# Optimization experiments

Hardware: AMD Instinct MI355X
Metric: run time of the kernel (lower is better)

## Reference

```python
import jax, jax.numpy as jnp
import numpy as np

V, B, N, D, L, H = 30522, 32, 512, 512, 4, 8
HD = D // H
REC = L // 2  # block-recurrent layer index
SCALE = HD ** -0.5


def _ln(x, g, b):
    m = x.mean(-1, keepdims=True)
    v = ((x - m) ** 2).mean(-1, keepdims=True)
    return (x - m) / jnp.sqrt(v + 1e-5) * g + b


def _rope(t):
    # t: [b,h,n,hd]; rotary embedding on token positions (split-half convention)
    n = t.shape[2]
    inv = 1.0 / (10000.0 ** (jnp.arange(0, HD, 2, dtype=jnp.float32) / HD))
    f = jnp.arange(n, dtype=jnp.float32)[:, None] * inv  # [n, hd/2]
    cos, sin = jnp.cos(f), jnp.sin(f)
    t1, t2 = t[..., : HD // 2], t[..., HD // 2 :]
    return jnp.concatenate([t1 * cos - t2 * sin, t2 * cos + t1 * sin], -1)


def _heads(x):
    b, n, _ = x.shape
    return x.reshape(b, n, H, HD).transpose(0, 2, 1, 3)


def _merge(x):
    b, h, n, d = x.shape
    return x.transpose(0, 2, 1, 3).reshape(b, n, h * d)


def _attn(q, k, v, mask):
    s = jnp.einsum('bhid,bhjd->bhij', q, k) * SCALE
    if mask is not None:
        s = jnp.where(mask, s, jnp.float32(-1e9))
    a = jax.nn.softmax(s, axis=-1)
    return jnp.einsum('bhij,bhjd->bhid', a, v)


def setup_inputs() -> dict:
    key = jax.random.key(0)
    ks = jax.random.split(key, 12)
    w = lambda k, shp: jax.random.normal(k, shp, jnp.float32) * 0.02
    return {
        'ids': jax.random.randint(ks[0], (B, N), 0, V),
        'state': jax.random.normal(ks[1], (B, D), jnp.float32),
        'tok_emb': w(ks[2], (V, D)),
        'ln1_g': jnp.ones((L, D), jnp.float32), 'ln1_b': jnp.zeros((L, D), jnp.float32),
        'w_qkv': w(ks[3], (L, D, 3 * D)),
        'w_o': w(ks[4], (L, D, D)),
        'ln2_g': jnp.ones((L, D), jnp.float32), 'ln2_b': jnp.zeros((L, D), jnp.float32),
        'w_ff1': w(ks[5], (L, D, 4 * D)), 'b_ff1': jnp.zeros((L, 4 * D), jnp.float32),
        'w_ff2': w(ks[6], (L, 4 * D, D)), 'b_ff2': jnp.zeros((L, D), jnp.float32),
        's_ln_g': jnp.ones((D,), jnp.float32), 's_ln_b': jnp.zeros((D,), jnp.float32),
        'w_s_qkv': w(ks[7], (D, 3 * D)),
        'w_so': w(ks[8], (D, D)),
        'gate_beta': w(ks[9], (D,)),
        'f_ln_g': jnp.ones((D,), jnp.float32), 'f_ln_b': jnp.zeros((D,), jnp.float32),
        'head_w': w(ks[10], (D, 1)), 'head_b': jnp.zeros((1,), jnp.float32),
    }


def reference(ids, state, tok_emb, ln1_g, ln1_b, w_qkv, w_o, ln2_g, ln2_b,
              w_ff1, b_ff1, w_ff2, b_ff2, s_ln_g, s_ln_b, w_s_qkv, w_so,
              gate_beta, f_ln_g, f_ln_b, head_w, head_b):
    x = tok_emb[ids]                       # [b,n,d]
    s = state[:, None, :]                  # [b,1,d]  (state.unsqueeze(1))
    n = x.shape[1]
    causal = jnp.tril(jnp.ones((n, n), bool))
    for l in range(L):
        h = _ln(x, ln1_g[l], ln1_b[l])
        q, k, v = jnp.split(h @ w_qkv[l], 3, axis=-1)
        q, k, v = _heads(q), _heads(k), _heads(v)
        q, k = _rope(q), _rope(k)
        if l == REC:
            sn = _ln(s, s_ln_g, s_ln_b)
            sq, sk, sv = jnp.split(sn @ w_s_qkv, 3, axis=-1)
            sq, sk, sv = _heads(sq), _heads(sk), _heads(sv)
            # tokens attend over [tokens (causal), state vector (always visible)]
            m = jnp.concatenate([causal, jnp.ones((n, 1), bool)], axis=1)
            out_x = _attn(q, jnp.concatenate([k, sk], 2), jnp.concatenate([v, sv], 2), m)
            x = x + _merge(out_x) @ w_o[l]
            # state attends over [state, all tokens] (no mask)
            out_s = _attn(sq, jnp.concatenate([sk, k], 2), jnp.concatenate([sv, v], 2), None)
            upd = _merge(out_s) @ w_so
            g = jax.nn.sigmoid(gate_beta)   # fixed learned-EMA gate
            s = s * g + upd * (1.0 - g)
        else:
            out_x = _attn(q, k, v, causal)
            x = x + _merge(out_x) @ w_o[l]
        h2 = _ln(x, ln2_g[l], ln2_b[l])
        x = x + jax.nn.gelu(h2 @ w_ff1[l] + b_ff1[l]) @ w_ff2[l] + b_ff2[l]
    x = _ln(x, f_ln_g, f_ln_b)
    state_out = s[:, 0, :]                 # state[0].squeeze()
    logits = x @ head_w + head_b           # [b,n,1]
    out = jax.nn.log_softmax(logits, axis=-1)
    return out, state_out
```

## Files before the change

kernel.cpp:

```cpp
#include <hip/hip_runtime.h>
#include <hip/hip_bf16.h>
#include <math.h>

#define B_ 32
#define N_ 512
#define D_ 512
#define H_ 8
#define HD_ 64
#define QKV_ 1536
#define SCALE_ 0.125f

typedef unsigned short u16;
typedef unsigned int u32;
typedef __attribute__((ext_vector_type(8))) short bf16x8;
typedef __attribute__((ext_vector_type(4))) float f32x4;

#define GLOBAL_AS __attribute__((address_space(1)))
#define LDS_AS __attribute__((address_space(3)))

__device__ __forceinline__ float gelu_f(float x) {
  float u = 0.7978845608028654f * (x + 0.044715f * x * x * x);
  u = fminf(fmaxf(u, -15.f), 15.f);
  float e = __expf(2.f * u);
  float th = 1.f - 2.f * __builtin_amdgcn_rcpf(e + 1.f);
  return 0.5f * x * (1.0f + th);
}

__device__ __forceinline__ u16 f2b(float f) {
  union { float f; u32 u; } v;
  v.f = f;
  u32 r = (v.u + 0x7FFFu + ((v.u >> 16) & 1u)) >> 16;
  return (u16)r;
}

__device__ __forceinline__ float b2f(u16 x) {
  union { u32 u; float f; } v;
  v.u = ((u32)x) << 16;
  return v.f;
}

__device__ __forceinline__ int xcd_swz(int orig, int nwg) {
  int q = nwg >> 3, r = nwg & 7;
  int xcd = orig & 7, idx = orig >> 3;
  return (xcd < r ? xcd * (q + 1) : r * (q + 1) + (xcd - r) * q) + idx;
}

__global__ void k_prep(const float* __restrict__ w_qkv, const float* __restrict__ w_o,
                       const float* __restrict__ w_ff1, const float* __restrict__ w_ff2,
                       u16* __restrict__ wq_t, u16* __restrict__ wo_t,
                       u16* __restrict__ wf1_t, u16* __restrict__ wf2_t,
                       float* __restrict__ out0, float2* __restrict__ tab) {
  __shared__ float tile[32][33];
  int bid = blockIdx.x;
  int t = threadIdx.x;
  if (bid < 64) {
    int idx = bid * 256 + t;
    out0[idx] = 0.f;
    int n = idx >> 5, i = idx & 31;
    float inv = powf(10000.0f, -(float)i * (1.0f / 32.0f));
    float f = (float)n * inv;
    float s, c;
    sincosf(f, &s, &c);
    tab[idx] = make_float2(c, s);
    return;
  }
  int b2 = bid - 64;
  const float* W;
  u16* Wt;
  int K, N;
  if (b2 < 2304) {
    int l = b2 / 768; b2 -= l * 768;
    W = w_qkv + (size_t)l * D_ * QKV_; Wt = wq_t + (size_t)l * QKV_ * D_;
    K = D_; N = QKV_;
  } else if (b2 < 2816) {
    b2 -= 2304; int l = b2 >> 8; b2 &= 255;
    W = w_o + (size_t)l * D_ * D_; Wt = wo_t + (size_t)l * D_ * D_;
    K = D_; N = D_;
  } else if (b2 < 4864) {
    b2 -= 2816; int l = b2 >> 10; b2 &= 1023;
    W = w_ff1 + (size_t)l * D_ * 4 * D_; Wt = wf1_t + (size_t)l * 4 * D_ * D_;
    K = D_; N = 4 * D_;
  } else {
    b2 -= 4864; int l = b2 >> 10; b2 &= 1023;
    W = w_ff2 + (size_t)l * 4 * D_ * D_; Wt = wf2_t + (size_t)l * D_ * 4 * D_;
    K = 4 * D_; N = D_;
  }
  int nbx = N >> 5;
  int bx = b2 % nbx, by = b2 / nbx;
  int k0 = by * 32, n0 = bx * 32;
  int r = t >> 3, c4 = (t & 7) * 4;
  float4 v = *(const float4*)&W[(size_t)(k0 + r) * N + n0 + c4];
  tile[r][c4] = v.x; tile[r][c4 + 1] = v.y; tile[r][c4 + 2] = v.z; tile[r][c4 + 3] = v.w;
  __syncthreads();
  ushort4 o;
  o.x = f2b(tile[c4 + 0][r]); o.y = f2b(tile[c4 + 1][r]);
  o.z = f2b(tile[c4 + 2][r]); o.w = f2b(tile[c4 + 3][r]);
  *(ushort4*)&Wt[(size_t)(n0 + r) * K + k0 + c4] = o;
}

__global__ void k_embed(const int* __restrict__ ids, const float* __restrict__ emb,
                        float* __restrict__ x) {
  int row = blockIdx.x;
  int id = ids[row];
  const float4* s = (const float4*)(emb + (size_t)id * D_);
  float4* d = (float4*)(x + (size_t)row * D_);
  d[threadIdx.x] = s[threadIdx.x];
}

template <int BF16OUT>
__global__ void k_ln(const float* __restrict__ in, const float* __restrict__ gw,
                     const float* __restrict__ bw, void* __restrict__ outv) {
  int row = blockIdx.x * 4 + (threadIdx.x >> 6);
  int lane = threadIdx.x & 63;
  const float* p = in + (size_t)row * D_ + lane * 8;
  float4 v0 = *(const float4*)p;
  float4 v1 = *(const float4*)(p + 4);
  float s = v0.x + v0.y + v0.z + v0.w + v1.x + v1.y + v1.z + v1.w;
  float q = v0.x * v0.x + v0.y * v0.y + v0.z * v0.z + v0.w * v0.w +
            v1.x * v1.x + v1.y * v1.y + v1.z * v1.z + v1.w * v1.w;
#pragma unroll
  for (int o = 32; o >= 1; o >>= 1) {
    s += __shfl_xor(s, o);
    q += __shfl_xor(q, o);
  }
  float mean = s * (1.0f / D_);
  float var = q * (1.0f / D_) - mean * mean;
  float rstd = rsqrtf(var + 1e-5f);
  float4 g0 = *(const float4*)(gw + lane * 8);
  float4 g1 = *(const float4*)(gw + lane * 8 + 4);
  float4 b0 = *(const float4*)(bw + lane * 8);
  float4 b1 = *(const float4*)(bw + lane * 8 + 4);
  float o8[8];
  o8[0] = (v0.x - mean) * rstd * g0.x + b0.x;
  o8[1] = (v0.y - mean) * rstd * g0.y + b0.y;
  o8[2] = (v0.z - mean) * rstd * g0.z + b0.z;
  o8[3] = (v0.w - mean) * rstd * g0.w + b0.w;
  o8[4] = (v1.x - mean) * rstd * g1.x + b1.x;
  o8[5] = (v1.y - mean) * rstd * g1.y + b1.y;
  o8[6] = (v1.z - mean) * rstd * g1.z + b1.z;
  o8[7] = (v1.w - mean) * rstd * g1.w + b1.w;
  if (BF16OUT) {
    u16* op = (u16*)outv + (size_t)row * D_ + lane * 8;
    ushort4 a, b;
    a.x = f2b(o8[0]); a.y = f2b(o8[1]); a.z = f2b(o8[2]); a.w = f2b(o8[3]);
    b.x = f2b(o8[4]); b.y = f2b(o8[5]); b.z = f2b(o8[6]); b.w = f2b(o8[7]);
    *(ushort4*)op = a;
    *(ushort4*)(op + 4) = b;
  } else {
    float* op = (float*)outv + (size_t)row * D_ + lane * 8;
    *(float4*)op = make_float4(o8[0], o8[1], o8[2], o8[3]);
    *(float4*)(op + 4) = make_float4(o8[4], o8[5], o8[6], o8[7]);
  }
}

template <int EPI, int BF16OUT>
__global__ __launch_bounds__(256) void k_mgemm(
    const u16* __restrict__ A, const u16* __restrict__ Bt,
    const float* __restrict__ bias, const float* __restrict__ resid,
    void* __restrict__ Cv, int M, int K, int Nc, int nb0) {
  __shared__ u16 As[2][128 * 32];
  __shared__ u16 Bs[2][128 * 32];
  int t = threadIdx.x;
  int wave = t >> 6, lane = t & 63;
  int nwg = gridDim.x * gridDim.y;
  int swz = xcd_swz(blockIdx.y * gridDim.x + blockIdx.x, nwg);
  int m0 = (swz / gridDim.x) * 128;
  int n0 = ((swz % gridDim.x) + nb0) * 128;
  int wr = wave >> 1, wc = wave & 1;
  f32x4 acc[4][4] = {};

  int srow = lane >> 2;
  int scol = ((lane & 3) ^ ((lane >> 3) & 3)) * 8;
  const u16* gaBase = A + (size_t)(m0 + wave * 32 + srow) * K + scol;
  const u16* gbBase = Bt + (size_t)(n0 + wave * 32 + srow) * K + scol;

#define STAGE_MG(bsel, kk)                                                     \
  {                                                                            \
    _Pragma("unroll") for (int i_ = 0; i_ < 2; ++i_) {                         \
      int rbase_ = wave * 32 + i_ * 16;                                        \
      __builtin_amdgcn_global_load_lds(                                        \
          (const GLOBAL_AS void*)(gaBase + (size_t)(i_ * 16) * K + (kk)),      \
          (LDS_AS void*)&As[bsel][rbase_ * 32], 16, 0, 0);                     \
      __builtin_amdgcn_global_load_lds(                                        \
          (const GLOBAL_AS void*)(gbBase + (size_t)(i_ * 16) * K + (kk)),      \
          (LDS_AS void*)&Bs[bsel][rbase_ * 32], 16, 0, 0);                     \
    }                                                                          \
  }

  int c = lane & 15, g = lane >> 4;
  int rsw = (c >> 1) & 3;
  int chread = (g ^ rsw) * 8;

  int nIter = K >> 5;
  STAGE_MG(0, 0);
  __syncthreads();
  for (int it = 0; it < nIter; ++it) {
    int cur = it & 1;
    if (it + 1 < nIter) STAGE_MG(cur ^ 1, (it + 1) << 5);
    const u16* as = As[cur];
    const u16* bs = Bs[cur];
    bf16x8 af[4], bfr[4];
#pragma unroll
    for (int mi = 0; mi < 4; ++mi)
      af[mi] = *(const bf16x8*)&as[(wr * 64 + mi * 16 + c) * 32 + chread];
#pragma unroll
    for (int ni = 0; ni < 4; ++ni)
      bfr[ni] = *(const bf16x8*)&bs[(wc * 64 + ni * 16 + c) * 32 + chread];
#pragma unroll
    for (int mi = 0; mi < 4; ++mi)
#pragma unroll
      for (int ni = 0; ni < 4; ++ni)
        acc[mi][ni] = __builtin_amdgcn_mfma_f32_16x16x32_bf16(bfr[ni], af[mi], acc[mi][ni], 0, 0, 0);
    __syncthreads();
  }
#undef STAGE_MG

#pragma unroll
  for (int mi = 0; mi < 4; ++mi) {
    int m = m0 + wr * 64 + mi * 16 + (lane & 15);
    size_t rowoff = (size_t)m * Nc;
#pragma unroll
    for (int ni = 0; ni < 4; ++ni) {
      int n = n0 + wc * 64 + ni * 16 + (lane >> 4) * 4;
      float v0 = acc[mi][ni][0], v1 = acc[mi][ni][1],
            v2 = acc[mi][ni][2], v3 = acc[mi][ni][3];
      if (EPI == 2 || EPI == 3) {
        float4 bb = *(const float4*)&bias[n];
        v0 += bb.x; v1 += bb.y; v2 += bb.z; v3 += bb.w;
      }
      if (EPI == 2) {
        v0 = gelu_f(v0); v1 = gelu_f(v1); v2 = gelu_f(v2); v3 = gelu_f(v3);
      }
      if (EPI == 1 || EPI == 3) {
        float4 rr = *(const float4*)&resid[rowoff + n];
        v0 += rr.x; v1 += rr.y; v2 += rr.z; v3 += rr.w;
      }
      if (BF16OUT) {
        ushort4 o;
        o.x = f2b(v0); o.y = f2b(v1); o.z = f2b(v2); o.w = f2b(v3);
        *(ushort4*)&((u16*)Cv)[rowoff + n] = o;
      } else {
        *(float4*)&((float*)Cv)[rowoff + n] = make_float4(v0, v1, v2, v3);
      }
    }
  }
}

template <int EPI>
__global__ __launch_bounds__(256) void k_gemm(const float* __restrict__ A,
                                              const float* __restrict__ W,
                                              const float* __restrict__ bias,
                                              const float* __restrict__ resid,
                                              float* __restrict__ C,
                                              int M, int K, int Nc) {
  __shared__ float As[32][68];
  __shared__ float Bs[32][68];
  int t = threadIdx.x;
  int tx = t & 15, ty = t >> 4;
  int m0 = blockIdx.y * 64, n0 = blockIdx.x * 64;
  float acc[4][4] = {};
  int ar = t >> 2, akc = (t & 3) * 8;
  int bkr = t >> 3, bnc = (t & 7) * 8;
  int garow = m0 + ar;
  bool aval = garow < M;
  const float* Aptr = A + (size_t)(aval ? garow : 0) * K + akc;
  const float* Wptr = W + (size_t)bkr * Nc + n0 + bnc;

  for (int k0 = 0; k0 < K; k0 += 32) {
    float4 a0, a1;
    if (aval) {
      a0 = *(const float4*)(Aptr + k0);
      a1 = *(const float4*)(Aptr + k0 + 4);
    } else {
      a0 = make_float4(0.f, 0.f, 0.f, 0.f);
      a1 = a0;
    }
    As[akc + 0][ar] = a0.x; As[akc + 1][ar] = a0.y;
    As[akc + 2][ar] = a0.z; As[akc + 3][ar] = a0.w;
    As[akc + 4][ar] = a1.x; As[akc + 5][ar] = a1.y;
    As[akc + 6][ar] = a1.z; As[akc + 7][ar] = a1.w;
    float4 b0 = *(const float4*)(Wptr + (size_t)k0 * Nc);
    float4 b1 = *(const float4*)(Wptr + (size_t)k0 * Nc + 4);
    *(float4*)&Bs[bkr][bnc] = b0;
    *(float4*)&Bs[bkr][bnc + 4] = b1;
    __syncthreads();
#pragma unroll
    for (int k = 0; k < 32; ++k) {
      float4 av = *(float4*)&As[k][ty * 4];
      float4 bv = *(float4*)&Bs[k][tx * 4];
      float a[4] = {av.x, av.y, av.z, av.w};
      float b[4] = {bv.x, bv.y, bv.z, bv.w};
#pragma unroll
      for (int i = 0; i < 4; ++i)
#pragma unroll
        for (int j = 0; j < 4; ++j) acc[i][j] += a[i] * b[j];
    }
    __syncthreads();
  }
#pragma unroll
  for (int i = 0; i < 4; ++i) {
    int m = m0 + ty * 4 + i;
    if (m >= M) break;
    size_t off = (size_t)m * Nc + n0 + tx * 4;
    float r[4];
#pragma unroll
    for (int j = 0; j < 4; ++j) {
      float v = acc[i][j];
      if (EPI == 2 || EPI == 3) v += bias[n0 + tx * 4 + j];
      if (EPI == 2) v = gelu_f(v);
      if (EPI == 1 || EPI == 3) v += resid[off + j];
      r[j] = v;
    }
    *(float4*)&C[off] = make_float4(r[0], r[1], r[2], r[3]);
  }
}

__global__ __launch_bounds__(512) void k_fattn(const u16* __restrict__ qkv,
                                               const float2* __restrict__ tab,
                                               u16* __restrict__ out) {
  __shared__ u16 Kl[64 * 64];
  __shared__ u16 Vt[64 * 64];
  __shared__ u16 Pl[8][16 * 64];
  int swz = xcd_swz(blockIdx.x, gridDim.x);
  int p = swz & 1, h = (swz >> 1) & 7, b = swz >> 4;
  int qtA = p, qtB = 3 - p;
  int t = threadIdx.x;
  int w = t >> 6, lane = t & 63;
  int c = lane & 15, g = lane >> 4;

  auto loadQ = [&](int qt, bf16x8* qa) {
    int n = qt * 128 + w * 16 + c;
    const u16* qptr = qkv + (size_t)(b * N_ + n) * QKV_ + h * HD_ + g * 8;
    union { bf16x8 v; u16 s[8]; } a0, a1, r0, r1;
    a0.v = *(const bf16x8*)qptr;
    a1.v = *(const bf16x8*)(qptr + 32);
    const float2* tb = tab + n * 32 + g * 8;
#pragma unroll
    for (int j = 0; j < 8; ++j) {
      float2 cs = tb[j];
      float lo = b2f(a0.s[j]), hi = b2f(a1.s[j]);
      r0.s[j] = f2b((lo * cs.x - hi * cs.y) * SCALE_);
      r1.s[j] = f2b((hi * cs.x + lo * cs.y) * SCALE_);
    }
    qa[0] = r0.v;
    qa[1] = r1.v;
  };

  bf16x8 qaA[2], qaB[2];
  loadQ(qtA, qaA);
  loadQ(qtB, qaB);

  f32x4 OA[4] = {}, OB[4] = {};
  float mA[4], lA[4], mB[4], lB[4];
#pragma unroll
  for (int r = 0; r < 4; ++r) { mA[r] = mB[r] = -1e30f; lA[r] = lB[r] = 0.f; }

  int myA = 2 * qtA + (w >> 2), myB = 2 * qtB + (w >> 2);
  int ktmax = 2 * qtB + 1;

  union { bf16x8 v; u16 s[8]; } rk0, rk1;
  ushort4 rv0a, rv0b, rv1a, rv1b;
  int krow = t >> 2, ki0 = (t & 3) * 8;
  int tt = t - 256, vkp = (tt >> 3) * 2, vd0 = (tt & 7) * 8;

  auto loadT = [&](int kt) {
    if (t < 256) {
      const u16* base = qkv + (size_t)(b * N_ + kt * 64 + krow) * QKV_ + D_ + h * HD_;
      rk0.v = *(const bf16x8*)(base + ki0);
      rk1.v = *(const bf16x8*)(base + ki0 + 32);
    } else {
      const u16* v0p = qkv + (size_t)(b * N_ + kt * 64 + vkp) * QKV_ + 2 * D_ + h * HD_ + vd0;
      const u16* v1p = v0p + QKV_;
      rv0a = *(const ushort4*)v0p;
      rv0b = *(const ushort4*)(v0p + 4);
      rv1a = *(const ushort4*)v1p;
      rv1b = *(const ushort4*)(v1p + 4);
    }
  };

  auto writeT = [&](int kt) {
    if (t < 256) {
      int n = kt * 64 + krow;
      const float2* tb = tab + n * 32 + ki0;
      union { bf16x8 v; u16 s[8]; } olo, ohi;
#pragma unroll
      for (int j = 0; j < 8; ++j) {
        float2 cs = tb[j];
        float fl = b2f(rk0.s[j]), fh = b2f(rk1.s[j]);
        olo.s[j] = f2b(fl * cs.x - fh * cs.y);
        ohi.s[j] = f2b(fh * cs.x + fl * cs.y);
      }
      int bb = krow * 128 + ki0 * 2, sw = (krow & 7) << 4;
      *(bf16x8*)((char*)Kl + (bb ^ sw)) = olo.v;
      *(bf16x8*)((char*)Kl + ((bb + 64) ^ sw)) = ohi.v;
    } else {
      u16 a0[8] = {rv0a.x, rv0a.y, rv0a.z, rv0a.w, rv0b.x, rv0b.y, rv0b.z, rv0b.w};
      u16 a1[8] = {rv1a.x, rv1a.y, rv1a.z, rv1a.w, rv1b.x, rv1b.y, rv1b.z, rv1b.w};
      u32* VtW = (u32*)Vt;
#pragma unroll
      for (int j = 0; j < 8; ++j) {
        int d = vd0 + j;
        VtW[(d * 32 + (vkp >> 1)) ^ ((d & 7) << 2)] = ((u32)a1[j] << 16) | (u32)a0[j];
      }
    }
  };

  auto compute = [&](const bf16x8* qa, f32x4* O, float* m_r, float* l_r,
                     int myblk, int qt, int kt) {
    f32x4 s[4] = {};
#pragma unroll
    for (int ks = 0; ks < 2; ++ks) {
#pragma unroll
      for (int nt = 0; nt < 4; ++nt) {
        int kr = nt * 16 + c;
        int byteoff = (kr * 128 + (g * 8 + ks * 32) * 2) ^ ((kr & 7) << 4);
        bf16x8 kb = *(const bf16x8*)((const char*)Kl + byteoff);
        s[nt] = __builtin_amdgcn_mfma_f32_16x16x32_bf16(qa[ks], kb, s[nt], 0, 0, 0);
      }
    }
    if (kt == myblk) {
#pragma unroll
      for (int nt = 0; nt < 4; ++nt)
#pragma unroll
        for (int r = 0; r < 4; ++r)
          if (kt * 64 + nt * 16 + c > qt * 128 + w * 16 + g * 4 + r) s[nt][r] = -1e30f;
    }
    float tm[4], tl[4], fac[4];
#pragma unroll
    for (int r = 0; r < 4; ++r)
      tm[r] = fmaxf(fmaxf(s[0][r], s[1][r]), fmaxf(s[2][r], s[3][r]));
#pragma unroll
    for (int msk = 1; msk <= 8; msk <<= 1)
#pragma unroll
      for (int r = 0; r < 4; ++r)
        tm[r] = fmaxf(tm[r], __shfl_xor(tm[r], msk));
#pragma unroll
    for (int r = 0; r < 4; ++r) {
      float mn = fmaxf(m_r[r], tm[r]);
      fac[r] = __expf(m_r[r] - mn);
      m_r[r] = mn;
      tl[r] = 0.f;
    }
    u16* plw = Pl[w];
#pragma unroll
    for (int nt = 0; nt < 4; ++nt) {
#pragma unroll
      for (int r = 0; r < 4; ++r) {
        float pv = __expf(s[nt][r] - m_r[r]);
        tl[r] += pv;
        int q = g * 4 + r, kk = nt * 16 + c;
        plw[(q * 64 + kk) ^ ((q & 7) << 3)] = f2b(pv);
      }
    }
#pragma unroll
    for (int msk = 1; msk <= 8; msk <<= 1)
#pragma unroll
      for (int r = 0; r < 4; ++r) tl[r] += __shfl_xor(tl[r], msk);
#pragma unroll
    for (int r = 0; r < 4; ++r) l_r[r] = l_r[r] * fac[r] + tl[r];
#pragma unroll
    for (int nt = 0; nt < 4; ++nt)
#pragma unroll
      for (int r = 0; r < 4; ++r) O[nt][r] *= fac[r];
#pragma unroll
    for (int ks = 0; ks < 2; ++ks) {
      int pbyte = (c * 128 + (g * 8 + ks * 32) * 2) ^ ((c & 7) << 4);
      bf16x8 pa = *(const bf16x8*)((const char*)plw + pbyte);
#pragma unroll
      for (int nt = 0; nt < 4; ++nt) {
        int d = nt * 16 + c;
        int vbyte = (d * 128 + (g * 8 + ks * 32) * 2) ^ ((d & 7) << 4);
        bf16x8 vb = *(const bf16x8*)((const char*)Vt + vbyte);
        O[nt] = __builtin_amdgcn_mfma_f32_16x16x32_bf16(pa, vb, O[nt], 0, 0, 0);
      }
    }
  };

  loadT(0);
  for (int kt = 0; kt <= ktmax; ++kt) {
    writeT(kt);
    __syncthreads();
    if (kt < ktmax) loadT(kt + 1);
    if (kt <= myA) compute(qaA, OA, mA, lA, myA, qtA, kt);
    if (kt <= myB) compute(qaB, OB, mB, lB, myB, qtB, kt);
    __syncthreads();
  }

  auto store = [&](int qt, const f32x4* O, const float* l_r) {
    u16* dst = out + (size_t)(b * N_ + qt * 128 + w * 16) * D_ + h * HD_;
#pragma unroll
    for (int nt = 0; nt < 4; ++nt) {
#pragma unroll
      for (int r = 0; r < 4; ++r) {
        int q = g * 4 + r;
        dst[(size_t)q * D_ + nt * 16 + c] = f2b(O[nt][r] / l_r[r]);
      }
    }
  };
  store(qtA, OA, lA);
  store(qtB, OB, lB);
}

__global__ __launch_bounds__(128) void k_state_attn(const float* __restrict__ sqkv,
                                                    const u16* __restrict__ qkv,
                                                    const float2* __restrict__ tab,
                                                    float* __restrict__ outs) {
  int h = blockIdx.x, b = blockIdx.y;
  __shared__ float sq[HD_];
  __shared__ float sc[513];
  __shared__ float red[128];
  int t = threadIdx.x;
  if (t < HD_) sq[t] = sqkv[(size_t)b * QKV_ + h * HD_ + t];
  __syncthreads();
  for (int j = t; j < 513; j += 128) {
    float acc = 0.f;
    if (j == 0) {
      const float* kp = sqkv + (size_t)b * QKV_ + D_ + h * HD_;
#pragma unroll
      for (int d = 0; d < HD_; ++d) acc += sq[d] * kp[d];
    } else {
      const u16* kp = qkv + (size_t)(b * N_ + j - 1) * QKV_ + D_ + h * HD_;
      const float2* tb = tab + (size_t)(j - 1) * 32;
#pragma unroll
      for (int d = 0; d < 32; ++d) {
        float2 cs = tb[d];
        float klo = b2f(kp[d]), khi = b2f(kp[d + 32]);
        acc += sq[d] * (klo * cs.x - khi * cs.y) + sq[d + 32] * (khi * cs.x + klo * cs.y);
      }
    }
    sc[j] = acc * SCALE_;
  }
  __syncthreads();
  float m = -1e30f;
  for (int j = t; j < 513; j += 128) m = fmaxf(m, sc[j]);
  red[t] = m;
  __syncthreads();
  for (int s = 64; s > 0; s >>= 1) {
    if (t < s) red[t] = fmaxf(red[t], red[t + s]);
    __syncthreads();
  }
  m = red[0];
  __syncthreads();
  float sum = 0.f;
  for (int j = t; j < 513; j += 128) {
    float p = expf(sc[j] - m);
    sc[j] = p;
    sum += p;
  }
  red[t] = sum;
  __syncthreads();
  for (int s = 64; s > 0; s >>= 1) {
    if (t < s) red[t] += red[t + s];
    __syncthreads();
  }
  float tot = red[0];
  if (t < HD_) {
    int d = t;
    float acc = sc[0] * sqkv[(size_t)b * QKV_ + 2 * D_ + h * HD_ + d];
    for (int j = 1; j <= N_; ++j)
      acc += sc[j] * b2f(qkv[(size_t)(b * N_ + j - 1) * QKV_ + 2 * D_ + h * HD_ + d]);
    outs[(size_t)b * D_ + h * HD_ + d] = acc / tot;
  }
}

__global__ void k_gate(const float* __restrict__ state, const float* __restrict__ upd,
                       const float* __restrict__ beta, float* __restrict__ out2) {
  int idx = blockIdx.x * 256 + threadIdx.x;
  int c = idx & (D_ - 1);
  float g = __builtin_amdgcn_rcpf(1.0f + __expf(-beta[c]));
  out2[idx] = state[idx] * g + upd[idx] * (1.0f - g);
}

extern "C" void kernel_launch(void* const* d_in, const int* in_sizes, int n_in,
                              void* d_out, int out_size, void* d_ws, size_t ws_size,
                              hipStream_t stream) {
  (void)in_sizes; (void)n_in; (void)out_size; (void)ws_size;
  const int* ids = (const int*)d_in[0];
  const float* state = (const float*)d_in[1];
  const float* tok_emb = (const float*)d_in[2];
  const float* ln1_g = (const float*)d_in[3];
  const float* ln1_b = (const float*)d_in[4];
  const float* w_qkv = (const float*)d_in[5];
  const float* w_o = (const float*)d_in[6];
  const float* ln2_g = (const float*)d_in[7];
  const float* ln2_b = (const float*)d_in[8];
  const float* w_ff1 = (const float*)d_in[9];
  const float* b_ff1 = (const float*)d_in[10];
  const float* w_ff2 = (const float*)d_in[11];
  const float* b_ff2 = (const float*)d_in[12];
  const float* s_ln_g = (const float*)d_in[13];
  const float* s_ln_b = (const float*)d_in[14];
  const float* w_s_qkv = (const float*)d_in[15];
  const float* w_so = (const float*)d_in[16];
  const float* gate_beta = (const float*)d_in[17];

  float* out0 = (float*)d_out;
  float* out1 = (float*)d_out + 16384;

  float* ws = (float*)d_ws;
  float* x = ws;
  u16* qkv_bf = (u16*)(ws + 8388608);
  u16* mid_bf = qkv_bf;
  u16* h_bf = (u16*)(ws + 25165824);
  u16* ao_bf = (u16*)(ws + 29360128);
  u16* wq_t = (u16*)(ws + 33554432);
  u16* wo_t = (u16*)(ws + 34734080);
  u16* wf1_t = (u16*)(ws + 34996224);
  u16* wf2_t = (u16*)(ws + 36044800);
  float* sln = ws + 37093376;
  float* sqkv = sln + 16384;
  float* souts = sqkv + 49152;
  float* supd = souts + 16384;
  float2* tab = (float2*)(ws + 37191680);

  const int M = B_ * N_;

  k_prep<<<dim3(6976), dim3(256), 0, stream>>>(w_qkv, w_o, w_ff1, w_ff2,
                                               wq_t, wo_t, wf1_t, wf2_t, out0, tab);
  k_embed<<<dim3(M), dim3(128), 0, stream>>>(ids, tok_emb, x);

  for (int l = 0; l < 3; ++l) {
    k_ln<1><<<dim3(M / 4), dim3(256), 0, stream>>>(x, ln1_g + l * D_, ln1_b + l * D_, h_bf);
    if (l == 2) {
      k_mgemm<0, 1><<<dim3(8, 128), dim3(256), 0, stream>>>(
          h_bf, wq_t + (size_t)l * QKV_ * D_, nullptr, nullptr, qkv_bf, M, D_, QKV_, 4);
      break;
    }
    k_mgemm<0, 1><<<dim3(12, 128), dim3(256), 0, stream>>>(
        h_bf, wq_t + (size_t)l * QKV_ * D_, nullptr, nullptr, qkv_bf, M, D_, QKV_, 0);
    k_fattn<<<dim3(2 * H_ * B_), dim3(512), 0, stream>>>(qkv_bf, tab, ao_bf);
    k_mgemm<1, 0><<<dim3(4, 128), dim3(256), 0, stream>>>(
        ao_bf, wo_t + (size_t)l * D_ * D_, nullptr, x, x, M, D_, D_, 0);
    k_ln<1><<<dim3(M / 4), dim3(256), 0, stream>>>(x, ln2_g + l * D_, ln2_b + l * D_, h_bf);
    k_mgemm<2, 1><<<dim3(16, 128), dim3(256), 0, stream>>>(
        h_bf, wf1_t + (size_t)l * 4 * D_ * D_, b_ff1 + l * 4 * D_, nullptr, mid_bf, M, D_, 4 * D_, 0);
    k_mgemm<3, 0><<<dim3(4, 128), dim3(256), 0, stream>>>(
        mid_bf, wf2_t + (size_t)l * D_ * 4 * D_, b_ff2 + l * D_, x, x, M, 4 * D_, D_, 0);
  }

  k_ln<0><<<dim3(B_ / 4), dim3(256), 0, stream>>>(state, s_ln_g, s_ln_b, sln);
  k_gemm<0><<<dim3(24, 1), dim3(256), 0, stream>>>(
      sln, w_s_qkv, nullptr, nullptr, sqkv, B_, D_, QKV_);
  k_state_attn<<<dim3(H_, B_), dim3(128), 0, stream>>>(sqkv, qkv_bf, tab, souts);
  k_gemm<0><<<dim3(8, 1), dim3(256), 0, stream>>>(
      souts, w_so, nullptr, nullptr, supd, B_, D_, D_);
  k_gate<<<dim3(64), dim3(256), 0, stream>>>(state, supd, gate_beta, out1);
}
```

Before: 648.0 us.

## Enlarge GEMM tiles to 256x256 with 8 waves and triple-buffered LDS pipeline

The bf16 MFMA GEMM now uses 256x256 output tiles with 512 threads, and each wave computes a 128x64 sub-tile. The double-buffered LDS staging becomes a three-stage pipeline that waits on explicit vmcnt counts and issues raw barriers, so global loads run two K-steps ahead. The aim is more reuse per loaded byte and better hiding of load latency. In exchange the kernel uses more LDS and registers and launches fewer workgroups, which can leave CUs idle on the small N=512 GEMMs.

```diff
diff --git a/kernel.cpp b/kernel.cpp
--- a/kernel.cpp
+++ b/kernel.cpp
@@ -154,70 +154,80 @@
 }
 
 template <int EPI, int BF16OUT>
-__global__ __launch_bounds__(256) void k_mgemm(
+__global__ __launch_bounds__(512) void k_mgemm(
     const u16* __restrict__ A, const u16* __restrict__ Bt,
     const float* __restrict__ bias, const float* __restrict__ resid,
     void* __restrict__ Cv, int M, int K, int Nc, int nb0) {
-  __shared__ u16 As[2][128 * 32];
-  __shared__ u16 Bs[2][128 * 32];
+  __shared__ u16 As[3][256 * 32];
+  __shared__ u16 Bs[3][256 * 32];
   int t = threadIdx.x;
-  int wave = t >> 6, lane = t & 63;
+  int w = t >> 6, lane = t & 63;
   int nwg = gridDim.x * gridDim.y;
   int swz = xcd_swz(blockIdx.y * gridDim.x + blockIdx.x, nwg);
-  int m0 = (swz / gridDim.x) * 128;
-  int n0 = ((swz % gridDim.x) + nb0) * 128;
-  int wr = wave >> 1, wc = wave & 1;
-  f32x4 acc[4][4] = {};
+  int m0 = (swz / gridDim.x) * 256;
+  int n0 = ((swz % gridDim.x) + nb0) * 256;
+  int wr = w >> 2, wc = w & 3;
+  f32x4 acc[8][4] = {};
 
   int srow = lane >> 2;
   int scol = ((lane & 3) ^ ((lane >> 3) & 3)) * 8;
-  const u16* gaBase = A + (size_t)(m0 + wave * 32 + srow) * K + scol;
-  const u16* gbBase = Bt + (size_t)(n0 + wave * 32 + srow) * K + scol;
+  const u16* gaBase = A + (size_t)(m0 + w * 32 + srow) * K + scol;
+  const u16* gbBase = Bt + (size_t)(n0 + w * 32 + srow) * K + scol;
 
 #define STAGE_MG(bsel, kk)                                                     \
   {                                                                            \
     _Pragma("unroll") for (int i_ = 0; i_ < 2; ++i_) {                         \
-      int rbase_ = wave * 32 + i_ * 16;                                        \
       __builtin_amdgcn_global_load_lds(                                        \
           (const GLOBAL_AS void*)(gaBase + (size_t)(i_ * 16) * K + (kk)),      \
-          (LDS_AS void*)&As[bsel][rbase_ * 32], 16, 0, 0);                     \
+          (LDS_AS void*)&As[bsel][(w * 32 + i_ * 16) * 32], 16, 0, 0);         \
       __builtin_amdgcn_global_load_lds(                                        \
           (const GLOBAL_AS void*)(gbBase + (size_t)(i_ * 16) * K + (kk)),      \
-          (LDS_AS void*)&Bs[bsel][rbase_ * 32], 16, 0, 0);                     \
+          (LDS_AS void*)&Bs[bsel][(w * 32 + i_ * 16) * 32], 16, 0, 0);         \
     }                                                                          \
   }
 
   int c = lane & 15, g = lane >> 4;
-  int rsw = (c >> 1) & 3;
-  int chread = (g ^ rsw) * 8;
-
-  int nIter = K >> 5;
+  int chread = (g ^ ((c >> 1) & 3)) * 8;
+
+  int nt = K >> 5;
   STAGE_MG(0, 0);
-  __syncthreads();
-  for (int it = 0; it < nIter; ++it) {
-    int cur = it & 1;
-    if (it + 1 < nIter) STAGE_MG(cur ^ 1, (it + 1) << 5);
+  STAGE_MG(1, 32);
+  asm volatile("s_waitcnt vmcnt(4)" ::: "memory");
+  __builtin_amdgcn_s_barrier();
+  asm volatile("" ::: "memory");
+
+  int cur = 0, nxt = 2;
+  for (int kt = 0; kt < nt; ++kt) {
+    if (kt + 2 < nt) STAGE_MG(nxt, (size_t)(kt + 2) << 5);
     const u16* as = As[cur];
     const u16* bs = Bs[cur];
-    bf16x8 af[4], bfr[4];
-#pragma unroll
-    for (int mi = 0; mi < 4; ++mi)
-      af[mi] = *(const bf16x8*)&as[(wr * 64 + mi * 16 + c) * 32 + chread];
+    bf16x8 bfr[4];
 #pragma unroll
     for (int ni = 0; ni < 4; ++ni)
       bfr[ni] = *(const bf16x8*)&bs[(wc * 64 + ni * 16 + c) * 32 + chread];
 #pragma unroll
-    for (int mi = 0; mi < 4; ++mi)
+    for (int mi = 0; mi < 8; ++mi) {
+      bf16x8 a = *(const bf16x8*)&as[(wr * 128 + mi * 16 + c) * 32 + chread];
 #pragma unroll
       for (int ni = 0; ni < 4; ++ni)
-        acc[mi][ni] = __builtin_amdgcn_mfma_f32_16x16x32_bf16(bfr[ni], af[mi], acc[mi][ni], 0, 0, 0);
-    __syncthreads();
+        acc[mi][ni] = __builtin_amdgcn_mfma_f32_16x16x32_bf16(bfr[ni], a, acc[mi][ni], 0, 0, 0);
+    }
+    if (kt + 1 < nt) {
+      if (kt + 2 < nt)
+        asm volatile("s_waitcnt vmcnt(4)" ::: "memory");
+      else
+        asm volatile("s_waitcnt vmcnt(0)" ::: "memory");
+      __builtin_amdgcn_s_barrier();
+      asm volatile("" ::: "memory");
+    }
+    cur = (cur + 1 == 3) ? 0 : cur + 1;
+    nxt = (nxt + 1 == 3) ? 0 : nxt + 1;
   }
 #undef STAGE_MG
 
 #pragma unroll
-  for (int mi = 0; mi < 4; ++mi) {
-    int m = m0 + wr * 64 + mi * 16 + (lane & 15);
+  for (int mi = 0; mi < 8; ++mi) {
+    int m = m0 + wr * 128 + mi * 16 + (lane & 15);
     size_t rowoff = (size_t)m * Nc;
 #pragma unroll
     for (int ni = 0; ni < 4; ++ni) {
@@ -622,19 +632,19 @@
   for (int l = 0; l < 3; ++l) {
     k_ln<1><<<dim3(M / 4), dim3(256), 0, stream>>>(x, ln1_g + l * D_, ln1_b + l * D_, h_bf);
     if (l == 2) {
-      k_mgemm<0, 1><<<dim3(8, 128), dim3(256), 0, stream>>>(
-          h_bf, wq_t + (size_t)l * QKV_ * D_, nullptr, nullptr, qkv_bf, M, D_, QKV_, 4);
+      k_mgemm<0, 1><<<dim3(4, 64), dim3(512), 0, stream>>>(
+          h_bf, wq_t + (size_t)l * QKV_ * D_, nullptr, nullptr, qkv_bf, M, D_, QKV_, 2);
       break;
     }
-    k_mgemm<0, 1><<<dim3(12, 128), dim3(256), 0, stream>>>(
+    k_mgemm<0, 1><<<dim3(6, 64), dim3(512), 0, stream>>>(
         h_bf, wq_t + (size_t)l * QKV_ * D_, nullptr, nullptr, qkv_bf, M, D_, QKV_, 0);
     k_fattn<<<dim3(2 * H_ * B_), dim3(512), 0, stream>>>(qkv_bf, tab, ao_bf);
-    k_mgemm<1, 0><<<dim3(4, 128), dim3(256), 0, stream>>>(
+    k_mgemm<1, 0><<<dim3(2, 64), dim3(512), 0, stream>>>(
         ao_bf, wo_t + (size_t)l * D_ * D_, nullptr, x, x, M, D_, D_, 0);
     k_ln<1><<<dim3(M / 4), dim3(256), 0, stream>>>(x, ln2_g + l * D_, ln2_b + l * D_, h_bf);
-    k_mgemm<2, 1><<<dim3(16, 128), dim3(256), 0, stream>>>(
+    k_mgemm<2, 1><<<dim3(8, 64), dim3(512), 0, stream>>>(
         h_bf, wf1_t + (size_t)l * 4 * D_ * D_, b_ff1 + l * 4 * D_, nullptr, mid_bf, M, D_, 4 * D_, 0);
-    k_mgemm<3, 0><<<dim3(4, 128), dim3(256), 0, stream>>>(
+    k_mgemm<3, 0><<<dim3(2, 64), dim3(512), 0, stream>>>(
         mid_bf, wf2_t + (size_t)l * D_ * 4 * D_, b_ff2 + l * D_, x, x, M, 4 * D_, D_, 0);
   }
 
```

Result: slower. 797.1 us (+23.0%).
